# Optimization experiments

Measured on AMD Instinct MI355X. Metric: run time of the kernel, lower is better.

The kernel has to match this reference:

```python
import jax, jax.numpy as jnp
import numpy as np
from jax import lax

B, S, C, L = 256, 30, 62, 169   # batch, timesteps, channels(nodes), data_seg
OG, OH = 64, 64                 # out_gcn, out_gru
K1, K2, K3 = 64, 32, 14         # depthwise kernel sizes (169-63-31-13 = 62 = C)


def setup_inputs() -> dict:
    key = jax.random.key(0)
    ks = jax.random.split(key, 26)
    def n(k, shape, s=0.05):
        return jax.random.normal(k, shape, dtype=jnp.float32) * s
    inp = {
        "x": jax.random.normal(ks[0], (B, S, C, L), dtype=jnp.float32),
        "adj": jax.random.normal(ks[1], (C, C), dtype=jnp.float32),
        # depthwise-separable conv 1 (kernel 64)
        "dw1_w": n(ks[2], (C, 1, K1)), "dw1_b": n(ks[3], (C,)),
        "pw1_w": n(ks[4], (C, C, 1)), "pw1_b": n(ks[5], (C,)),
        # depthwise-separable conv 2 (kernel 32)
        "dw2_w": n(ks[6], (C, 1, K2)), "dw2_b": n(ks[7], (C,)),
        "pw2_w": n(ks[8], (C, C, 1)), "pw2_b": n(ks[9], (C,)),
        # depthwise-separable conv 3 (kernel 14)
        "dw3_w": n(ks[10], (C, 1, K3)), "dw3_b": n(ks[11], (C,)),
        "pw3_w": n(ks[12], (C, C, 1)), "pw3_b": n(ks[13], (C,)),
        # GraphConvolution(data_seg, out_gcn): support = x @ W; out = adj @ support + b
        "gcn_w": n(ks[14], (L, OG)), "gcn_b": n(ks[15], (OG,)),
        # GRU-style gate Linears (out_gcn+out_gru -> out_gru), torch layout (out, in)
        "Wr_w": n(ks[16], (OH, OG + OH)), "Wr_b": n(ks[17], (OH,)),
        "Wu_w": n(ks[18], (OH, OG + OH)), "Wu_b": n(ks[19], (OH,)),
        "Wc_w": n(ks[20], (OH, OG + OH)), "Wc_b": n(ks[21], (OH,)),
        # extra learned gate biases b_r/b_u/b_c (init zeros in torch)
        "b_r": jnp.zeros((OH,), jnp.float32),
        "b_u": jnp.zeros((OH,), jnp.float32),
        "b_c": jnp.zeros((OH,), jnp.float32),
    }
    return inp


def _dsconv(x, dw, dwb, pw, pwb):
    # x: (b, c, l); depthwise (groups=c, valid padding) then pointwise 1x1
    dn = ("NCH", "OIH", "NCH")
    y = lax.conv_general_dilated(x, dw, (1,), "VALID", dimension_numbers=dn,
                                 feature_group_count=x.shape[1]) + dwb[None, :, None]
    y = lax.conv_general_dilated(y, pw, (1,), "VALID", dimension_numbers=dn) + pwb[None, :, None]
    return y


def reference(x, adj, dw1_w, dw1_b, pw1_w, pw1_b, dw2_w, dw2_b, pw2_w, pw2_b,
              dw3_w, dw3_b, pw3_w, pw3_b, gcn_w, gcn_b,
              Wr_w, Wr_b, Wu_w, Wu_b, Wc_w, Wc_b, b_r, b_u, b_c):
    b, s, c, l = x.shape
    oh = b_r.shape[0]

    def step(h, xt):            # h: (b*c, oh), xt: (b, c, l)
        d = _dsconv(xt, dw1_w, dw1_b, pw1_w, pw1_b)
        d = _dsconv(d, dw2_w, dw2_b, pw2_w, pw2_b)
        d = _dsconv(d, dw3_w, dw3_b, pw3_w, pw3_b)      # (b, c, c)
        adj_t = jax.nn.sigmoid(d + adj)                  # adaptive adjacency
        support = jnp.einsum("bcl,lf->bcf", xt, gcn_w)
        g = jnp.einsum("bij,bjf->bif", adj_t, support) + gcn_b  # (b, c, og)
        gf = g.reshape(b * c, -1)
        cat = jnp.concatenate([gf, h], axis=-1)
        r = jax.nn.sigmoid(cat @ Wr_w.T + Wr_b + b_r)
        u = jax.nn.sigmoid(cat @ Wu_w.T + Wu_b + b_u)
        cc = jnp.tanh(jnp.concatenate([gf, r * h], axis=-1) @ Wc_w.T + Wc_b + b_c)
        h_new = u * h + (1.0 - u) * cc
        return h_new, None

    h0 = jnp.zeros((b * c, oh), x.dtype)
    xs = jnp.swapaxes(x, 0, 1)          # (s, b, c, l)
    h_last, _ = lax.scan(step, h0, xs)
    return h_last.reshape(b, c, oh)[:, -1, :]   # (b, out_gru)
```

## Files before the change

kernel.cpp:

```cpp
#include <hip/hip_runtime.h>
#include <math.h>

#define BB 256
#define SS 30
#define CC 62
#define LL 169
#define OG 64
#define OH 64
#define KK1 64
#define KK2 32
#define KK3 14
#define FLEN 108

typedef __attribute__((ext_vector_type(8))) short s16x8;
typedef __attribute__((ext_vector_type(4))) float f32x4;

__device__ __forceinline__ unsigned short f2bf(float f) {
    unsigned u = __float_as_uint(f);
    u += 0x7fffu + ((u >> 16) & 1u);
    return (unsigned short)(u >> 16);
}
__device__ __forceinline__ float bflo(unsigned v) { return __uint_as_float(v << 16); }
__device__ __forceinline__ float bfhi(unsigned v) { return __uint_as_float(v & 0xffff0000u); }

__device__ __forceinline__ void gload_lds4(const void* g, void* l) {
    __builtin_amdgcn_global_load_lds(
        (const __attribute__((address_space(1))) void*)g,
        (__attribute__((address_space(3))) void*)l, 4, 0, 0);
}
__device__ __forceinline__ void gload_lds16(const void* g, void* l) {
    __builtin_amdgcn_global_load_lds(
        (const __attribute__((address_space(1))) void*)g,
        (__attribute__((address_space(3))) void*)l, 16, 0, 0);
}

__global__ __launch_bounds__(1024) void k_setup1(
        const float* __restrict__ dw1, const float* __restrict__ dw1b,
        const float* __restrict__ pw1, const float* __restrict__ pw1b,
        const float* __restrict__ dw2, const float* __restrict__ dw2b,
        const float* __restrict__ pw2, const float* __restrict__ pw2b,
        const float* __restrict__ dw3, const float* __restrict__ dw3b,
        const float* __restrict__ pw3, const float* __restrict__ pw3b,
        const float* __restrict__ Wr, const float* __restrict__ Wrb, const float* __restrict__ br,
        const float* __restrict__ Wu, const float* __restrict__ Wub, const float* __restrict__ bu,
        const float* __restrict__ Wc, const float* __restrict__ Wcb, const float* __restrict__ bc,
        float* __restrict__ Bmg, float* __restrict__ WtAll,
        float* __restrict__ bias192, float* __restrict__ beff) {
    __shared__ float g23[CC * KK3];
    __shared__ float Am[CC * 45];
    __shared__ float by2[CC], vals[CC];
    int tid = threadIdx.x;

    for (int idx = tid; idx < OG * 192; idx += 1024) {
        int i = idx / 192, q = idx - i * 192;
        int gate = q >> 6, f = q & 63;
        const float* W = gate == 0 ? Wr : (gate == 1 ? Wu : Wc);
        WtAll[idx] = W[f * (OG + OH) + i];
    }
    if (tid < 192) {
        int gate = tid >> 6, f = tid & 63;
        const float* Wb = gate == 0 ? Wrb : (gate == 1 ? Wub : Wcb);
        const float* bb = gate == 0 ? br  : (gate == 1 ? bu  : bc);
        bias192[tid] = Wb[f] + bb[f];
    }
    for (int idx = tid; idx < CC * KK3; idx += 1024) {
        int c1 = idx / KK3, k3 = idx - c1 * KK3;
        float s = 0.f;
        for (int c2 = 0; c2 < CC; ++c2)
            s += pw3[61 * CC + c2] * pw2[c2 * CC + c1] * dw3[c2 * KK3 + k3];
        g23[idx] = s;
    }
    if (tid < CC) {
        int c1 = tid;
        float bz1 = pw1b[c1];
        for (int c0 = 0; c0 < CC; ++c0) bz1 += pw1[c1 * CC + c0] * dw1b[c0];
        float s2 = 0.f;
        for (int k = 0; k < KK2; ++k) s2 += dw2[c1 * KK2 + k];
        by2[c1] = dw2b[c1] + bz1 * s2;
    }
    __syncthreads();
    if (tid < CC) {
        int c2 = tid;
        float bz2 = pw2b[c2];
        for (int c1 = 0; c1 < CC; ++c1) bz2 += pw2[c2 * CC + c1] * by2[c1];
        float s3 = 0.f;
        for (int k = 0; k < KK3; ++k) s3 += dw3[c2 * KK3 + k];
        vals[c2] = pw3[61 * CC + c2] * (dw3b[c2] + bz2 * s3);
    }
    for (int idx = tid; idx < CC * 45; idx += 1024) {
        int c1 = idx / 45, m = idx - c1 * 45;
        int k2lo = max(0, m - (KK3 - 1));
        int k2hi = min(KK2 - 1, m);
        float s = 0.f;
        for (int k2 = k2lo; k2 <= k2hi; ++k2)
            s += dw2[c1 * KK2 + k2] * g23[c1 * KK3 + (m - k2)];
        Am[idx] = s;
    }
    __syncthreads();
    if (tid == 0) {
        float s = pw3b[61];
        for (int c2 = 0; c2 < CC; ++c2) s += vals[c2];
        *beff = s;
    }
    for (int idx = tid; idx < CC * 45; idx += 1024) {
        int c0 = idx / 45, m = idx - c0 * 45;
        float s = 0.f;
        for (int c1 = 0; c1 < CC; ++c1) s += pw1[c1 * CC + c0] * Am[c1 * 45 + m];
        Bmg[idx] = s;
    }
}

__global__ __launch_bounds__(128) void k_setupF(
        const float* __restrict__ Bmg, const float* __restrict__ dw1,
        unsigned short* __restrict__ Ftb) {
    __shared__ float Bl[45];
    int c0 = blockIdx.x;
    int o = threadIdx.x;
    if (c0 < CC && o < 45) Bl[o] = Bmg[c0 * 45 + o];
    __syncthreads();
    if (o >= 112) return;
    float s = 0.f;
    if (c0 < CC && o < FLEN) {
        int mlo = max(0, o - (KK1 - 1));
        int mhi = min(44, o);
        for (int m = mlo; m <= mhi; ++m)
            s += Bl[m] * dw1[c0 * KK1 + (o - m)];
    }
    Ftb[o * 64 + c0] = f2bf(s);
}

__global__ __launch_bounds__(256, 2) void k_main(
        const float* __restrict__ x, const float* __restrict__ adj,
        const unsigned short* __restrict__ Ftb, const float* __restrict__ beff_p,
        float* __restrict__ wxb) {
    __shared__ __align__(16) unsigned xf32[10480];
    __shared__ __align__(16) unsigned short xT[176 * 64];
    __shared__ float dacc[4][64];
    __shared__ float adjt[CC];
    int bt = blockIdx.x;
    int tid = threadIdx.x;
    int lane = tid & 63, wid = tid >> 6;
    const char* xgb = (const char*)x + (size_t)bt * 41912;
    unsigned* xTu = (unsigned*)xT;

    int par = bt & 1;
    int off = par ? 8 : 0;
    #pragma unroll
    for (int it = 0; it < 11; ++it) {
        int ch = it * 256 + tid;
        if (ch < 2619)
            gload_lds16(xgb + off + (size_t)ch * 16,
                        (char*)xf32 + off + it * 4096 + wid * 1024);
    }
    {
        int ed = par ? 0 : 10476;
        if (tid < 2)
            gload_lds4(xgb + (size_t)(ed + tid) * 4, (char*)xf32 + (size_t)ed * 4);
    }
    float be = *beff_p;
    float arow = 0.f;
    if (tid < CC) arow = adj[61 * CC + tid];
    int col = lane & 15, rb4 = lane >> 4;
    const unsigned short* ap0 = Ftb + ((wid * 16 + col) * 64 + rb4 * 8);
    s16x8 pa0 = *(const s16x8*)ap0;
    s16x8 pa1 = *(const s16x8*)(ap0 + 32);
    int mt2c = wid + 4 < 7 ? wid + 4 : 6;
    const unsigned short* ap1 = Ftb + ((mt2c * 16 + col) * 64 + rb4 * 8);
    s16x8 pb0 = *(const s16x8*)ap1;
    s16x8 pb1 = *(const s16x8*)(ap1 + 32);
    ((float*)dacc)[tid] = 0.f;
    for (int i = tid; i < 169; i += 256) xTu[(i * 32 + 31) ^ ((i & 7) << 2)] = 0;
    for (int i = tid; i < 224; i += 256) {
        int r = 169 + (i >> 5), d2 = i & 31;
        xTu[(r * 32 + d2) ^ ((r & 7) << 2)] = 0;
    }
    __syncthreads();

    for (int idx = tid; idx < 31 * 169; idx += 256) {
        int l = idx / 31, cp = idx - l * 31;
        unsigned lo = xf32[(2 * cp) * 169 + l];
        unsigned hi = xf32[(2 * cp + 1) * 169 + l];
        unsigned v = (unsigned)f2bf(__uint_as_float(lo))
                   | ((unsigned)f2bf(__uint_as_float(hi)) << 16);
        xTu[(l * 32 + cp) ^ ((l & 7) << 2)] = v;
    }
    __syncthreads();

    f32x4 zacc[5];
    #pragma unroll
    for (int d = 0; d < 5; ++d) zacc[d] = (f32x4){0.f, 0.f, 0.f, 0.f};
    int kb = rb4 * 16;
    int xr = (lane & 7) << 4;
    #pragma unroll
    for (int h = 0; h < 2; ++h) {
        int mt = wid + 4 * h;
        if (mt < 7) {
            s16x8 a0 = h == 0 ? pa0 : pb0;
            s16x8 a1 = h == 0 ? pa1 : pb1;
            #pragma unroll
            for (int d = 0; d < 5; ++d) {
                int nt = mt + d;
                int bbyte = ((nt * 16 + col) * 128 + kb) ^ xr;
                s16x8 b0 = *(const s16x8*)((const char*)xT + bbyte);
                s16x8 b1 = *(const s16x8*)((const char*)xT + bbyte + 64);
                zacc[d] = __builtin_amdgcn_mfma_f32_16x16x32_bf16(a0, b0, zacc[d], 0, 0, 0);
                zacc[d] = __builtin_amdgcn_mfma_f32_16x16x32_bf16(a1, b1, zacc[d], 0, 0, 0);
            }
        }
    }
    int jc = col - rb4 * 4;
    #pragma unroll
    for (int d = 0; d < 5; ++d) {
        #pragma unroll
        for (int r = 0; r < 4; ++r) {
            int j = 16 * d + jc - r;
            if ((unsigned)j < 62u) atomicAdd(&dacc[rb4][j], zacc[d][r]);
        }
    }
    __syncthreads();

    if (tid < CC) {
        float dv = dacc[0][tid] + dacc[1][tid] + dacc[2][tid] + dacc[3][tid];
        adjt[tid] = 1.f / (1.f + __expf(-(dv + be + arow)));
    }
    __syncthreads();

    if (tid < 176) {
        float s = 0.f;
        if (tid < LL) {
            #pragma unroll 2
            for (int j = 0; j < CC; ++j)
                s += adjt[j] * __uint_as_float(xf32[j * LL + tid]);
        }
        wxb[(size_t)bt * 176 + tid] = s;
    }
}

__global__ __launch_bounds__(256) void k_gg(
        const float* __restrict__ wxb, const float* __restrict__ gcnw,
        const float* __restrict__ gcnb, const float* __restrict__ WtAll,
        const float* __restrict__ bias192, float* __restrict__ gates) {
    __shared__ float wxl[8 * 176];
    __shared__ float Gl[8 * 64];
    int bt0 = blockIdx.x * 8;
    int tid = threadIdx.x;
    const float* src = wxb + (size_t)bt0 * 176;
    for (int i = tid; i < 8 * 176; i += 256) wxl[i] = src[i];
    __syncthreads();
    #pragma unroll
    for (int rep = 0; rep < 2; ++rep) {
        int i = rep * 256 + tid;
        int bl = i >> 6, f = i & 63;
        float s = gcnb[f];
        const float* wr = wxl + bl * 176;
        #pragma unroll 13
        for (int l = 0; l < LL; ++l) s += wr[l] * gcnw[l * OG + f];
        Gl[i] = s;
    }
    __syncthreads();
    float* gout = gates + (size_t)bt0 * 192;
    #pragma unroll
    for (int rep = 0; rep < 6; ++rep) {
        int i = rep * 256 + tid;
        int bl = i / 192, q = i - bl * 192;
        const float* gr = Gl + bl * 64;
        float s = bias192[q];
        #pragma unroll 16
        for (int k = 0; k < OG; ++k) s += gr[k] * WtAll[k * 192 + q];
        gout[i] = s;
    }
}

__global__ __launch_bounds__(256) void k_scan(
        const float* __restrict__ gates,
        const float* __restrict__ Wr, const float* __restrict__ Wu, const float* __restrict__ Wc,
        float* __restrict__ out) {
    __shared__ float hl[OH], rhl[OH];
    int b = blockIdx.x;
    int tid = threadIdx.x;
    int f = tid >> 2, q = tid & 3;
    float wr[16], wu[16], wc[16];
    #pragma unroll
    for (int i = 0; i < 16; ++i) {
        int col = OG + q * 16 + i;
        wr[i] = Wr[f * (OG + OH) + col];
        wu[i] = Wu[f * (OG + OH) + col];
        wc[i] = Wc[f * (OG + OH) + col];
    }
    float h = 0.f;
    if (tid < OH) hl[tid] = 0.f;
    __syncthreads();
    for (int t = 0; t < SS; ++t) {
        const float* gp = gates + ((size_t)b * SS + t) * 192;
        float gr = gp[f];
        float gu = gp[64 + f];
        float gc = gp[128 + f];
        float rv = 0.f, uv = 0.f;
        #pragma unroll
        for (int i = 0; i < 16; ++i) {
            float hv = hl[q * 16 + i];
            rv += wr[i] * hv;
            uv += wu[i] * hv;
        }
        rv += __shfl_xor(rv, 1); rv += __shfl_xor(rv, 2);
        uv += __shfl_xor(uv, 1); uv += __shfl_xor(uv, 2);
        float r = 1.f / (1.f + __expf(-(rv + gr)));
        float u = 1.f / (1.f + __expf(-(uv + gu)));
        if (q == 0) rhl[f] = r * h;
        __syncthreads();
        float cv = 0.f;
        #pragma unroll
        for (int i = 0; i < 16; ++i) cv += wc[i] * rhl[q * 16 + i];
        cv += __shfl_xor(cv, 1); cv += __shfl_xor(cv, 2);
        float cc = tanhf(cv + gc);
        if (q == 0) {
            h = u * h + (1.f - u) * cc;
            hl[f] = h;
        }
        __syncthreads();
    }
    if (q == 0) out[b * OH + f] = h;
}

extern "C" void kernel_launch(void* const* d_in, const int* in_sizes, int n_in,
                              void* d_out, int out_size, void* d_ws, size_t ws_size,
                              hipStream_t stream) {
    const float* x    = (const float*)d_in[0];
    const float* adj  = (const float*)d_in[1];
    const float* dw1w = (const float*)d_in[2];
    const float* dw1b = (const float*)d_in[3];
    const float* pw1w = (const float*)d_in[4];
    const float* pw1b = (const float*)d_in[5];
    const float* dw2w = (const float*)d_in[6];
    const float* dw2b = (const float*)d_in[7];
    const float* pw2w = (const float*)d_in[8];
    const float* pw2b = (const float*)d_in[9];
    const float* dw3w = (const float*)d_in[10];
    const float* dw3b = (const float*)d_in[11];
    const float* pw3w = (const float*)d_in[12];
    const float* pw3b = (const float*)d_in[13];
    const float* gcnw = (const float*)d_in[14];
    const float* gcnb = (const float*)d_in[15];
    const float* Wrw  = (const float*)d_in[16];
    const float* Wrb  = (const float*)d_in[17];
    const float* Wuw  = (const float*)d_in[18];
    const float* Wub  = (const float*)d_in[19];
    const float* Wcw  = (const float*)d_in[20];
    const float* Wcb  = (const float*)d_in[21];
    const float* br   = (const float*)d_in[22];
    const float* bu   = (const float*)d_in[23];
    const float* bc   = (const float*)d_in[24];
    float* out = (float*)d_out;

    char* ws = (char*)d_ws;
    unsigned short* Ftb = (unsigned short*)(ws + 0);
    float* WtAll        = (float*)(ws + 14336);
    float* bias192      = (float*)(ws + 63488);
    float* beff         = (float*)(ws + 64256);
    float* Bmg          = (float*)(ws + 64320);
    float* wxb          = (float*)(ws + 76800);
    float* gates        = (float*)(ws + 5483520);
    (void)ws_size; (void)in_sizes; (void)n_in; (void)out_size;

    k_setup1<<<1, 1024, 0, stream>>>(dw1w, dw1b, pw1w, pw1b, dw2w, dw2b, pw2w, pw2b,
                                     dw3w, dw3b, pw3w, pw3b,
                                     Wrw, Wrb, br, Wuw, Wub, bu, Wcw, Wcb, bc,
                                     Bmg, WtAll, bias192, beff);
    k_setupF<<<64, 128, 0, stream>>>(Bmg, dw1w, Ftb);
    k_main<<<BB * SS, 256, 0, stream>>>(x, adj, Ftb, beff, wxb);
    k_gg<<<BB * SS / 8, 256, 0, stream>>>(wxb, gcnw, gcnb, WtAll, bias192, gates);
    k_scan<<<BB, 256, 0, stream>>>(gates, Wrw, Wuw, Wcw, out);
}
```

Baseline: 346.1 us.

## Make k_main persistent over 15 slices with double-buffered async loads

k_main now processes 15 (batch,timestep) slices per block. Each slice is split into three chunks that stream through a two-buffer LDS ring using global_load_lds, overlapping the load of later chunks with the bf16 transpose and MFMA work on the current one. The final adj-weighted reduction now reads the bf16 transposed copy instead of the fp32 buffer. This lowers precision for that sum and adds manual waitcnt/barrier bookkeeping, which is easy to get wrong. Launching fewer blocks cuts per-block setup and lets memory traffic hide behind compute.

```diff
diff --git a/kernel.cpp b/kernel.cpp
--- a/kernel.cpp
+++ b/kernel.cpp
@@ -11,6 +11,8 @@
 #define KK2 32
 #define KK3 14
 #define FLEN 108
+#define NT 15
+#define NSTEP (3 * NT)
 
 typedef __attribute__((ext_vector_type(8))) short s16x8;
 typedef __attribute__((ext_vector_type(4))) float f32x4;
@@ -32,6 +34,31 @@
     __builtin_amdgcn_global_load_lds(
         (const __attribute__((address_space(1))) void*)g,
         (__attribute__((address_space(3))) void*)l, 16, 0, 0);
+}
+
+__device__ __forceinline__ void issue_step(const char* gb, char* lb, int n3, int tid) {
+    int shb = (int)((size_t)gb & 8);
+    int sh  = shb >> 2;
+    int q   = n3 - sh;
+    int nch = q >> 2;
+    int rem = q & 3;
+    int wofs = (tid >> 6) * 1024;
+    #pragma unroll
+    for (int r = 0; r < 4; ++r) {
+        int cc = r * 256 + tid;
+        if (cc > nch - 1) cc = nch - 1;
+        gload_lds16(gb + shb + (size_t)cc * 16, lb + 2 * shb + r * 4096 + wofs);
+    }
+    if (tid < 2) {
+        if (sh) gload_lds4(gb + 4 * tid, lb + 8);
+        else    gload_lds4(gb + 4 * tid, lb + 16400);
+        if (rem) {
+            int g0 = sh + 4 * nch;
+            gload_lds4(gb + 4 * (g0 + tid), lb + 4 * (g0 + sh));
+        } else {
+            gload_lds4(gb + 4 * tid, lb + 16408);
+        }
+    }
 }
 
 __global__ __launch_bounds__(1024) void k_setup1(
@@ -133,34 +160,27 @@
         const float* __restrict__ x, const float* __restrict__ adj,
         const unsigned short* __restrict__ Ftb, const float* __restrict__ beff_p,
         float* __restrict__ wxb) {
-    __shared__ __align__(16) unsigned xf32[10480];
+    __shared__ __align__(16) char fbuf[2][16416];
     __shared__ __align__(16) unsigned short xT[176 * 64];
     __shared__ float dacc[4][64];
-    __shared__ float adjt[CC];
-    int bt = blockIdx.x;
+    __shared__ float adjt[64];
+
     int tid = threadIdx.x;
     int lane = tid & 63, wid = tid >> 6;
-    const char* xgb = (const char*)x + (size_t)bt * 41912;
+    int col = lane & 15, rb4 = lane >> 4;
     unsigned* xTu = (unsigned*)xT;
 
-    int par = bt & 1;
-    int off = par ? 8 : 0;
-    #pragma unroll
-    for (int it = 0; it < 11; ++it) {
-        int ch = it * 256 + tid;
-        if (ch < 2619)
-            gload_lds16(xgb + off + (size_t)ch * 16,
-                        (char*)xf32 + off + it * 4096 + wid * 1024);
-    }
-    {
-        int ed = par ? 0 : 10476;
-        if (tid < 2)
-            gload_lds4(xgb + (size_t)(ed + tid) * 4, (char*)xf32 + (size_t)ed * 4);
-    }
+    const int off3[3]  = {0, 13520, 28392};
+    const int n3tab[3] = {3380, 3718, 3380};
+    const int cp0tab[3] = {0, 10, 21};
+    const int ncptab[3] = {10, 11, 10};
+
+    const char* xblk = (const char*)x + (size_t)blockIdx.x * NT * 41912;
+
+    for (int i = tid; i < 176 * 32; i += 256) xTu[i] = 0;
+    ((float*)dacc)[tid & 255] = 0.f;
     float be = *beff_p;
-    float arow = 0.f;
-    if (tid < CC) arow = adj[61 * CC + tid];
-    int col = lane & 15, rb4 = lane >> 4;
+    float arow = (tid < CC) ? adj[61 * CC + tid] : 0.f;
     const unsigned short* ap0 = Ftb + ((wid * 16 + col) * 64 + rb4 * 8);
     s16x8 pa0 = *(const s16x8*)ap0;
     s16x8 pa1 = *(const s16x8*)(ap0 + 32);
@@ -168,71 +188,108 @@
     const unsigned short* ap1 = Ftb + ((mt2c * 16 + col) * 64 + rb4 * 8);
     s16x8 pb0 = *(const s16x8*)ap1;
     s16x8 pb1 = *(const s16x8*)(ap1 + 32);
-    ((float*)dacc)[tid] = 0.f;
-    for (int i = tid; i < 169; i += 256) xTu[(i * 32 + 31) ^ ((i & 7) << 2)] = 0;
-    for (int i = tid; i < 224; i += 256) {
-        int r = 169 + (i >> 5), d2 = i & 31;
-        xTu[(r * 32 + d2) ^ ((r & 7) << 2)] = 0;
-    }
-    __syncthreads();
-
-    for (int idx = tid; idx < 31 * 169; idx += 256) {
-        int l = idx / 31, cp = idx - l * 31;
-        unsigned lo = xf32[(2 * cp) * 169 + l];
-        unsigned hi = xf32[(2 * cp + 1) * 169 + l];
-        unsigned v = (unsigned)f2bf(__uint_as_float(lo))
-                   | ((unsigned)f2bf(__uint_as_float(hi)) << 16);
-        xTu[(l * 32 + cp) ^ ((l & 7) << 2)] = v;
-    }
-    __syncthreads();
-
-    f32x4 zacc[5];
-    #pragma unroll
-    for (int d = 0; d < 5; ++d) zacc[d] = (f32x4){0.f, 0.f, 0.f, 0.f};
+
+    issue_step(xblk + off3[0], fbuf[0], n3tab[0], tid);
+    issue_step(xblk + off3[1], fbuf[1], n3tab[1], tid);
+    asm volatile("s_waitcnt lgkmcnt(0)" ::: "memory");
+    __builtin_amdgcn_sched_barrier(0);
+
     int kb = rb4 * 16;
     int xr = (lane & 7) << 4;
-    #pragma unroll
-    for (int h = 0; h < 2; ++h) {
-        int mt = wid + 4 * h;
-        if (mt < 7) {
-            s16x8 a0 = h == 0 ? pa0 : pb0;
-            s16x8 a1 = h == 0 ? pa1 : pb1;
+    int jc = col - rb4 * 4;
+
+    for (int k = 0; k < NSTEP; ++k) {
+        int th = k % 3;
+        int t = k / 3;
+        if (k == NSTEP - 1)      { asm volatile("s_waitcnt vmcnt(0)" ::: "memory"); }
+        else if (wid == 0)       { asm volatile("s_waitcnt vmcnt(6)" ::: "memory"); }
+        else                     { asm volatile("s_waitcnt vmcnt(4)" ::: "memory"); }
+        __builtin_amdgcn_sched_barrier(0);
+        __builtin_amdgcn_s_barrier();
+
+        {
+            const char* gb = xblk + (size_t)t * 41912 + off3[th];
+            int sh = ((int)((size_t)gb & 8)) >> 2;
+            const unsigned* fb = (const unsigned*)fbuf[k & 1];
+            int ncp = ncptab[th], cp0 = cp0tab[th];
+            for (int it = tid; it < 16 * 169; it += 256) {
+                int cpL = it & 15, l = it >> 4;
+                if (cpL < ncp) {
+                    int glo = (2 * cpL) * 169 + l;
+                    unsigned lo = fb[glo + sh];
+                    unsigned hi = fb[glo + 169 + sh];
+                    unsigned v = (unsigned)f2bf(__uint_as_float(lo))
+                               | ((unsigned)f2bf(__uint_as_float(hi)) << 16);
+                    xTu[(l * 32 + cp0 + cpL) ^ ((l & 7) << 2)] = v;
+                }
+            }
+        }
+        asm volatile("s_waitcnt lgkmcnt(0)" ::: "memory");
+        __builtin_amdgcn_sched_barrier(0);
+        __builtin_amdgcn_s_barrier();
+
+        if (k + 2 < NSTEP) {
+            int k2 = k + 2, th2 = k2 % 3, t2 = k2 / 3;
+            issue_step(xblk + (size_t)t2 * 41912 + off3[th2], fbuf[k & 1], n3tab[th2], tid);
+        }
+
+        if (th == 2) {
+            f32x4 zacc[5];
+            #pragma unroll
+            for (int d = 0; d < 5; ++d) zacc[d] = (f32x4){0.f, 0.f, 0.f, 0.f};
+            #pragma unroll
+            for (int h = 0; h < 2; ++h) {
+                int mt = wid + 4 * h;
+                if (mt < 7) {
+                    s16x8 a0 = h == 0 ? pa0 : pb0;
+                    s16x8 a1 = h == 0 ? pa1 : pb1;
+                    #pragma unroll
+                    for (int d = 0; d < 5; ++d) {
+                        int nt = mt + d;
+                        int bbyte = ((nt * 16 + col) * 128 + kb) ^ xr;
+                        s16x8 b0 = *(const s16x8*)((const char*)xT + bbyte);
+                        s16x8 b1 = *(const s16x8*)((const char*)xT + bbyte + 64);
+                        zacc[d] = __builtin_amdgcn_mfma_f32_16x16x32_bf16(a0, b0, zacc[d], 0, 0, 0);
+                        zacc[d] = __builtin_amdgcn_mfma_f32_16x16x32_bf16(a1, b1, zacc[d], 0, 0, 0);
+                    }
+                }
+            }
             #pragma unroll
             for (int d = 0; d < 5; ++d) {
-                int nt = mt + d;
-                int bbyte = ((nt * 16 + col) * 128 + kb) ^ xr;
-                s16x8 b0 = *(const s16x8*)((const char*)xT + bbyte);
-                s16x8 b1 = *(const s16x8*)((const char*)xT + bbyte + 64);
-                zacc[d] = __builtin_amdgcn_mfma_f32_16x16x32_bf16(a0, b0, zacc[d], 0, 0, 0);
-                zacc[d] = __builtin_amdgcn_mfma_f32_16x16x32_bf16(a1, b1, zacc[d], 0, 0, 0);
+                #pragma unroll
+                for (int r = 0; r < 4; ++r) {
+                    int j = 16 * d + jc - r;
+                    if ((unsigned)j < 62u) atomicAdd(&dacc[rb4][j], zacc[d][r]);
+                }
             }
-        }
-    }
-    int jc = col - rb4 * 4;
-    #pragma unroll
-    for (int d = 0; d < 5; ++d) {
-        #pragma unroll
-        for (int r = 0; r < 4; ++r) {
-            int j = 16 * d + jc - r;
-            if ((unsigned)j < 62u) atomicAdd(&dacc[rb4][j], zacc[d][r]);
-        }
-    }
-    __syncthreads();
-
-    if (tid < CC) {
-        float dv = dacc[0][tid] + dacc[1][tid] + dacc[2][tid] + dacc[3][tid];
-        adjt[tid] = 1.f / (1.f + __expf(-(dv + be + arow)));
-    }
-    __syncthreads();
-
-    if (tid < 176) {
-        float s = 0.f;
-        if (tid < LL) {
-            #pragma unroll 2
-            for (int j = 0; j < CC; ++j)
-                s += adjt[j] * __uint_as_float(xf32[j * LL + tid]);
-        }
-        wxb[(size_t)bt * 176 + tid] = s;
+            asm volatile("s_waitcnt lgkmcnt(0)" ::: "memory");
+            __builtin_amdgcn_sched_barrier(0);
+            __builtin_amdgcn_s_barrier();
+
+            if (tid < CC) {
+                float dv = dacc[0][tid] + dacc[1][tid] + dacc[2][tid] + dacc[3][tid];
+                adjt[tid] = 1.f / (1.f + __expf(-(dv + be + arow)));
+                dacc[0][tid] = 0.f; dacc[1][tid] = 0.f;
+                dacc[2][tid] = 0.f; dacc[3][tid] = 0.f;
+            }
+            asm volatile("s_waitcnt lgkmcnt(0)" ::: "memory");
+            __builtin_amdgcn_sched_barrier(0);
+            __builtin_amdgcn_s_barrier();
+
+            if (tid < 176) {
+                float s = 0.f;
+                if (tid < LL) {
+                    int xorv = (tid & 7) << 2;
+                    #pragma unroll
+                    for (int m = 0; m < 31; ++m) {
+                        unsigned v = xTu[(tid * 32 + m) ^ xorv];
+                        s += adjt[2 * m] * bflo(v) + adjt[2 * m + 1] * bfhi(v);
+                    }
+                }
+                wxb[((size_t)(blockIdx.x * NT + t)) * 176 + tid] = s;
+            }
+            __builtin_amdgcn_s_barrier();
+        }
     }
 }
 
@@ -367,7 +424,7 @@
                                      Wrw, Wrb, br, Wuw, Wub, bu, Wcw, Wcb, bc,
                                      Bmg, WtAll, bias192, beff);
     k_setupF<<<64, 128, 0, stream>>>(Bmg, dw1w, Ftb);
-    k_main<<<BB * SS, 256, 0, stream>>>(x, adj, Ftb, beff, wxb);
+    k_main<<<BB * SS / NT, 256, 0, stream>>>(x, adj, Ftb, beff, wxb);
     k_gg<<<BB * SS / 8, 256, 0, stream>>>(wxb, gcnw, gcnb, WtAll, bias192, gates);
     k_scan<<<BB, 256, 0, stream>>>(gates, Wrw, Wuw, Wcw, out);
 }
```

After: 353.8 us. +2.2%, slower.
